# Performance work log

Measured on AMD Instinct MI355X. Metric: run time of the kernel, lower is better.

Reference implementation:

```python
import jax, jax.numpy as jnp
import numpy as np

N_NODES = 50000


def gcn_conv(x, src, dst, W, b):
    # PyG GCNConv: x @ W, symmetric gcn_norm with self-loops, scatter-add, + bias
    n = x.shape[0]
    x = x @ W  # [N, out]
    deg = jax.ops.segment_sum(jnp.ones_like(src, dtype=x.dtype), dst, num_segments=n)
    dinv = jnp.where(deg > 0, deg ** -0.5, 0.0)
    norm = dinv[src] * dinv[dst]  # [E+N]
    out = jax.ops.segment_sum(x[src] * norm[:, None], dst, num_segments=n)
    return out + b


def setup_inputs() -> dict:
    key = jax.random.key(0)
    ks = jax.random.split(key, 8)
    x = jax.random.normal(ks[0], (N_NODES, 128), dtype=jnp.float32)
    edge_index = jax.random.randint(ks[1], (2, 800000), 0, N_NODES, dtype=jnp.int64)
    def glorot(k, fan_in, fan_out):
        s = (6.0 / (fan_in + fan_out)) ** 0.5
        return jax.random.uniform(k, (fan_in, fan_out), jnp.float32, -s, s)
    return {
        "x": x,
        "edge_index": edge_index,
        "W1": glorot(ks[2], 128, 128), "b1": jnp.zeros((128,), jnp.float32),
        "W2": glorot(ks[3], 128, 128), "b2": jnp.zeros((128,), jnp.float32),
        "W3": glorot(ks[4], 128, 64), "b3": jnp.zeros((64,), jnp.float32),
    }


def reference(x, edge_index, W1, b1, W2, b2, W3, b3):
    n = x.shape[0]
    loops = jnp.arange(n, dtype=edge_index.dtype)
    src = jnp.concatenate([edge_index[0], loops])  # self-loops appended
    dst = jnp.concatenate([edge_index[1], loops])
    h = gcn_conv(x, src, dst, W1, b1)
    h = jax.nn.relu(h)  # dropout is identity in eval mode
    h = gcn_conv(h, src, dst, W2, b2)
    h = jax.nn.relu(h)
    h = gcn_conv(h, src, dst, W3, b3)
    return h
```

## Files before the change

kernel.cpp:

```cpp
#include <hip/hip_runtime.h>
#include <hip/hip_bf16.h>
#include <hip/hip_fp16.h>


typedef __attribute__((ext_vector_type(8))) short s16x8;
typedef __attribute__((ext_vector_type(8))) unsigned short u16x8;
typedef __attribute__((ext_vector_type(4))) float f32x4;

__device__ __forceinline__ float bfu_lo(uint v) { return __uint_as_float(v << 16); }
__device__ __forceinline__ float bfu_hi(uint v) { return __uint_as_float(v & 0xffff0000u); }
__device__ __forceinline__ float dec_norm(uint m) {
    return __half2float(__ushort_as_half((ushort)(m >> 16)));
}
__device__ __forceinline__ ushort bf16_bits(float f) {
    union { __hip_bfloat16 h; ushort u; } x;
    x.h = __float2bfloat16(f);
    return x.u;
}


__global__ void k_init(int* __restrict__ deg, int n,
                       uint4* __restrict__ ep4, int cap4) {
    int i = blockIdx.x * blockDim.x + threadIdx.x;
    if (i < n) deg[i] = 1;
    if (i < cap4) ep4[i] = make_uint4(0u, 0u, 0u, 0u);
}

__global__ void k_hist(const int* __restrict__ dst, int E,
                       int* __restrict__ deg, ushort* __restrict__ rank) {
    int e = blockIdx.x * blockDim.x + threadIdx.x;
    if (e < E) {
        int r = atomicAdd(&deg[dst[e]], 1);
        rank[e] = (ushort)r;
    }
}

__global__ void k_scan_block(const int* __restrict__ deg, int* __restrict__ offs,
                             int* __restrict__ bsum, float* __restrict__ dinv, int n) {
    __shared__ int sm[256];
    int tid = threadIdx.x;
    int i = blockIdx.x * 256 + tid;
    int v = (i < n) ? deg[i] : 0;
    int pv = (i < n) ? ((v + 7) & ~7) : 0;
    if (i < n) dinv[i] = rsqrtf((float)v);
    sm[tid] = pv;
    __syncthreads();
    for (int off = 1; off < 256; off <<= 1) {
        int t = (tid >= off) ? sm[tid - off] : 0;
        __syncthreads();
        sm[tid] += t;
        __syncthreads();
    }
    if (i < n) offs[i] = sm[tid] - pv;
    if (tid == 255) bsum[blockIdx.x] = sm[255];
}

__global__ void k_scan_bsum(int* __restrict__ bsum, int nb, int* __restrict__ offs, int n) {
    __shared__ int sm[256];
    int tid = threadIdx.x;
    int v = (tid < nb) ? bsum[tid] : 0;
    sm[tid] = v;
    __syncthreads();
    for (int off = 1; off < 256; off <<= 1) {
        int t = (tid >= off) ? sm[tid - off] : 0;
        __syncthreads();
        sm[tid] += t;
        __syncthreads();
    }
    if (tid < nb) bsum[tid] = sm[tid] - v;
    if (tid == 255) offs[n] = sm[255];
}

__global__ void k_add_bsum(int* __restrict__ offs, const int* __restrict__ bsum, int n) {
    int i = blockIdx.x * blockDim.x + threadIdx.x;
    if (i < n) offs[i] += bsum[i >> 8];
}

__global__ __launch_bounds__(256) void k_fill(const int* __restrict__ src,
                                              const int* __restrict__ dst,
                                              const ushort* __restrict__ rank,
                                              int E, int n,
                                              const int* __restrict__ offs,
                                              const float* __restrict__ dinv,
                                              uint* __restrict__ ep) {
    int e = blockIdx.x * blockDim.x + threadIdx.x;
    int tot = E + n;
    if (e >= tot) return;
    int s, d, r;
    if (e < E) {
        s = src[e];
        d = dst[e];
        r = rank[e];
    } else {
        s = d = e - E;
        r = 0;
    }
    int pos = offs[d] + r;
    uint hb = (uint)__half_as_ushort(__float2half(dinv[s] * dinv[d]));
    ep[pos] = (hb << 16) | (uint)s;
}

__global__ void k_transW(const float* __restrict__ W1, const float* __restrict__ W2,
                         ushort* __restrict__ Wt1, ushort* __restrict__ Wt2) {
    int i = blockIdx.x * 256 + threadIdx.x;
    if (i < 128 * 128) {
        int r = i >> 7, c = i & 127;
        Wt1[c * 128 + r] = bf16_bits(W1[i]);
        Wt2[c * 128 + r] = bf16_bits(W2[i]);
    }
}

template <bool ABF16>
__global__ __launch_bounds__(256) void k_gemm_mfma(const void* __restrict__ Ain,
                                                   const ushort* __restrict__ Wt,
                                                   __hip_bfloat16* __restrict__ T, int n) {
    __shared__ ushort As[64][136];
    __shared__ ushort Ws[128][136];
    const int tid = threadIdx.x;
    const int wave = tid >> 6, lane = tid & 63;
    const int m0 = blockIdx.x * 64;

#pragma unroll
    for (int it = 0; it < 8; ++it) {
        int idx = it * 256 + tid;
        int r = idx >> 4;
        int c8 = (idx & 15) << 3;
        *(u16x8*)&Ws[r][c8] = *(const u16x8*)(Wt + r * 128 + c8);
    }
    if constexpr (ABF16) {
        const ushort* A = (const ushort*)Ain;
#pragma unroll
        for (int it = 0; it < 4; ++it) {
            int idx = it * 256 + tid;
            int r = idx >> 4;
            int c8 = (idx & 15) << 3;
            u16x8 v = {0, 0, 0, 0, 0, 0, 0, 0};
            if (m0 + r < n) v = *(const u16x8*)(A + (size_t)(m0 + r) * 128 + c8);
            *(u16x8*)&As[r][c8] = v;
        }
    } else {
        const float* A = (const float*)Ain;
#pragma unroll
        for (int it = 0; it < 8; ++it) {
            int idx = it * 256 + tid;
            int r = idx >> 5;
            int c4 = (idx & 31) << 2;
            float4 v = make_float4(0.f, 0.f, 0.f, 0.f);
            if (m0 + r < n) v = *(const float4*)(A + (size_t)(m0 + r) * 128 + c4);
            As[r][c4 + 0] = bf16_bits(v.x);
            As[r][c4 + 1] = bf16_bits(v.y);
            As[r][c4 + 2] = bf16_bits(v.z);
            As[r][c4 + 3] = bf16_bits(v.w);
        }
    }
    __syncthreads();

    const int lrow = lane & 15;
    const int kgrp = lane >> 4;

    s16x8 a[4];
#pragma unroll
    for (int kk = 0; kk < 4; ++kk)
        a[kk] = *(const s16x8*)&As[wave * 16 + lrow][kk * 32 + kgrp * 8];

    f32x4 acc[8];
#pragma unroll
    for (int nt = 0; nt < 8; ++nt) {
        f32x4 c = {0.f, 0.f, 0.f, 0.f};
#pragma unroll
        for (int kk = 0; kk < 4; ++kk) {
            s16x8 b = *(const s16x8*)&Ws[nt * 16 + lrow][kk * 32 + kgrp * 8];
            c = __builtin_amdgcn_mfma_f32_16x16x32_bf16(a[kk], b, c, 0, 0, 0);
        }
        acc[nt] = c;
    }

    ushort* To = (ushort*)T;
#pragma unroll
    for (int j = 0; j < 4; ++j) {
        int row = m0 + wave * 16 + kgrp * 4 + j;
        if (row < n) {
#pragma unroll
            for (int nt = 0; nt < 8; ++nt)
                To[(size_t)row * 128 + nt * 16 + lrow] = bf16_bits(acc[nt][j]);
        }
    }
}

__global__ __launch_bounds__(256) void k_gemm64(const ushort* __restrict__ Aq,
                                                const float* __restrict__ W,
                                                __hip_bfloat16* __restrict__ T, int n) {
    __shared__ float As[32][68];
    __shared__ float Bs[32][68];
    const int tid = threadIdx.x;
    const int tx = tid & 15, ty = tid >> 4;
    const int m0 = blockIdx.x * 64;

    float acc[4][4] = {};

    for (int k0 = 0; k0 < 128; k0 += 32) {
#pragma unroll
        for (int it = 0; it < 2; ++it) {
            int idx = it * 256 + tid;
            int r = idx >> 3;
            int c4 = (idx & 7) << 2;
            float4 v = make_float4(0.f, 0.f, 0.f, 0.f);
            if (m0 + r < n) {
                ushort4 u = *(const ushort4*)(Aq + (size_t)(m0 + r) * 128 + k0 + c4);
                v.x = __uint_as_float((uint)u.x << 16);
                v.y = __uint_as_float((uint)u.y << 16);
                v.z = __uint_as_float((uint)u.z << 16);
                v.w = __uint_as_float((uint)u.w << 16);
            }
            As[c4 + 0][r] = v.x;
            As[c4 + 1][r] = v.y;
            As[c4 + 2][r] = v.z;
            As[c4 + 3][r] = v.w;
        }
#pragma unroll
        for (int it = 0; it < 2; ++it) {
            int idx = it * 256 + tid;
            int kk = idx >> 4;
            int c4 = (idx & 15) << 2;
            *(float4*)&Bs[kk][c4] = *(const float4*)(W + (size_t)(k0 + kk) * 64 + c4);
        }
        __syncthreads();

#pragma unroll
        for (int k = 0; k < 32; ++k) {
            float4 a = *(const float4*)&As[k][ty * 4];
            float4 b0 = *(const float4*)&Bs[k][tx * 4];
            float av[4] = {a.x, a.y, a.z, a.w};
#pragma unroll
            for (int i = 0; i < 4; ++i) {
                acc[i][0] += av[i] * b0.x;
                acc[i][1] += av[i] * b0.y;
                acc[i][2] += av[i] * b0.z;
                acc[i][3] += av[i] * b0.w;
            }
        }
        __syncthreads();
    }

#pragma unroll
    for (int i = 0; i < 4; ++i) {
        int r = m0 + ty * 4 + i;
        if (r < n) {
            union { ushort h[4]; uint2 u; } p;
#pragma unroll
            for (int j = 0; j < 4; ++j) p.h[j] = bf16_bits(acc[i][j]);
            *(uint2*)((ushort*)T + (size_t)r * 64 + tx * 4) = p.u;
        }
    }
}

template <bool RELU>
__global__ __launch_bounds__(256) void k_agg128(const __hip_bfloat16* __restrict__ T,
                                                const int* __restrict__ offs,
                                                const uint* __restrict__ ep,
                                                const float* __restrict__ bias,
                                                uint* __restrict__ outq, int n) {
    int pr = blockIdx.x * 4 + (threadIdx.x >> 6);
    int lane = threadIdx.x & 63;
    int w0 = pr * 2;
    if (w0 >= n) return;
    int w1 = w0 + 1;
    bool has1 = (w1 < n);
    int eA = offs[w0], endA = offs[w0 + 1];
    int eB = has1 ? offs[w1] : 0;
    int endB = has1 ? offs[w1 + 1] : 0;

    const uint* Tl = (const uint*)T + lane;
    const uint4 z4 = make_uint4(0u, 0u, 0u, 0u);
    float a0 = 0.f, a1 = 0.f, c0 = 0.f, c1 = 0.f;

    uint4 mA0 = *(const uint4*)(ep + eA);
    uint4 mA1 = *(const uint4*)(ep + eA + 4);
    uint4 mB0 = z4, mB1 = z4;
    if (eB < endB) { mB0 = *(const uint4*)(ep + eB); mB1 = *(const uint4*)(ep + eB + 4); }

    for (;;) {
        uint rA0 = Tl[(size_t)(mA0.x & 0xffffu) * 64];
        uint rA1 = Tl[(size_t)(mA0.y & 0xffffu) * 64];
        uint rA2 = Tl[(size_t)(mA0.z & 0xffffu) * 64];
        uint rA3 = Tl[(size_t)(mA0.w & 0xffffu) * 64];
        uint rA4 = Tl[(size_t)(mA1.x & 0xffffu) * 64];
        uint rA5 = Tl[(size_t)(mA1.y & 0xffffu) * 64];
        uint rA6 = Tl[(size_t)(mA1.z & 0xffffu) * 64];
        uint rA7 = Tl[(size_t)(mA1.w & 0xffffu) * 64];
        uint rB0 = Tl[(size_t)(mB0.x & 0xffffu) * 64];
        uint rB1 = Tl[(size_t)(mB0.y & 0xffffu) * 64];
        uint rB2 = Tl[(size_t)(mB0.z & 0xffffu) * 64];
        uint rB3 = Tl[(size_t)(mB0.w & 0xffffu) * 64];
        uint rB4 = Tl[(size_t)(mB1.x & 0xffffu) * 64];
        uint rB5 = Tl[(size_t)(mB1.y & 0xffffu) * 64];
        uint rB6 = Tl[(size_t)(mB1.z & 0xffffu) * 64];
        uint rB7 = Tl[(size_t)(mB1.w & 0xffffu) * 64];
        float wA0 = dec_norm(mA0.x), wA1 = dec_norm(mA0.y);
        float wA2 = dec_norm(mA0.z), wA3 = dec_norm(mA0.w);
        float wA4 = dec_norm(mA1.x), wA5 = dec_norm(mA1.y);
        float wA6 = dec_norm(mA1.z), wA7 = dec_norm(mA1.w);
        float wB0 = dec_norm(mB0.x), wB1 = dec_norm(mB0.y);
        float wB2 = dec_norm(mB0.z), wB3 = dec_norm(mB0.w);
        float wB4 = dec_norm(mB1.x), wB5 = dec_norm(mB1.y);
        float wB6 = dec_norm(mB1.z), wB7 = dec_norm(mB1.w);
        eA += 8;
        eB += 8;
        bool moreA = (eA < endA), moreB = (eB < endB);
        if (moreA) { mA0 = *(const uint4*)(ep + eA); mA1 = *(const uint4*)(ep + eA + 4); }
        else       { mA0 = z4; mA1 = z4; }
        if (moreB) { mB0 = *(const uint4*)(ep + eB); mB1 = *(const uint4*)(ep + eB + 4); }
        else       { mB0 = z4; mB1 = z4; }
        a0 += wA0 * bfu_lo(rA0); a1 += wA0 * bfu_hi(rA0);
        a0 += wA1 * bfu_lo(rA1); a1 += wA1 * bfu_hi(rA1);
        a0 += wA2 * bfu_lo(rA2); a1 += wA2 * bfu_hi(rA2);
        a0 += wA3 * bfu_lo(rA3); a1 += wA3 * bfu_hi(rA3);
        a0 += wA4 * bfu_lo(rA4); a1 += wA4 * bfu_hi(rA4);
        a0 += wA5 * bfu_lo(rA5); a1 += wA5 * bfu_hi(rA5);
        a0 += wA6 * bfu_lo(rA6); a1 += wA6 * bfu_hi(rA6);
        a0 += wA7 * bfu_lo(rA7); a1 += wA7 * bfu_hi(rA7);
        c0 += wB0 * bfu_lo(rB0); c1 += wB0 * bfu_hi(rB0);
        c0 += wB1 * bfu_lo(rB1); c1 += wB1 * bfu_hi(rB1);
        c0 += wB2 * bfu_lo(rB2); c1 += wB2 * bfu_hi(rB2);
        c0 += wB3 * bfu_lo(rB3); c1 += wB3 * bfu_hi(rB3);
        c0 += wB4 * bfu_lo(rB4); c1 += wB4 * bfu_hi(rB4);
        c0 += wB5 * bfu_lo(rB5); c1 += wB5 * bfu_hi(rB5);
        c0 += wB6 * bfu_lo(rB6); c1 += wB6 * bfu_hi(rB6);
        c0 += wB7 * bfu_lo(rB7); c1 += wB7 * bfu_hi(rB7);
        if (!moreA && !moreB) break;
    }

    float2 b = *(const float2*)(bias + (lane << 1));
    a0 += b.x; a1 += b.y;
    if (RELU) { a0 = fmaxf(a0, 0.f); a1 = fmaxf(a1, 0.f); }
    outq[(size_t)w0 * 64 + lane] = ((uint)bf16_bits(a1) << 16) | (uint)bf16_bits(a0);
    if (has1) {
        c0 += b.x; c1 += b.y;
        if (RELU) { c0 = fmaxf(c0, 0.f); c1 = fmaxf(c1, 0.f); }
        outq[(size_t)w1 * 64 + lane] = ((uint)bf16_bits(c1) << 16) | (uint)bf16_bits(c0);
    }
}

__global__ __launch_bounds__(256) void k_agg64(const __hip_bfloat16* __restrict__ T,
                                               const int* __restrict__ offs,
                                               const uint* __restrict__ ep,
                                               const float* __restrict__ bias,
                                               float* __restrict__ out, int n) {
    int pr = blockIdx.x * 4 + (threadIdx.x >> 6);
    int lane = threadIdx.x & 63;
    int w0 = pr * 2;
    if (w0 >= n) return;
    int w1 = w0 + 1;
    bool has1 = (w1 < n);
    int eA = offs[w0], endA = offs[w0 + 1];
    int eB = has1 ? offs[w1] : 0;
    int endB = has1 ? offs[w1 + 1] : 0;

    const ushort* Tl = (const ushort*)T + lane;
    const uint4 z4 = make_uint4(0u, 0u, 0u, 0u);
    float a0 = 0.f, c0 = 0.f;

    uint4 mA0 = *(const uint4*)(ep + eA);
    uint4 mA1 = *(const uint4*)(ep + eA + 4);
    uint4 mB0 = z4, mB1 = z4;
    if (eB < endB) { mB0 = *(const uint4*)(ep + eB); mB1 = *(const uint4*)(ep + eB + 4); }

    for (;;) {
        float rA0 = __uint_as_float((uint)Tl[(size_t)(mA0.x & 0xffffu) * 64] << 16);
        float rA1 = __uint_as_float((uint)Tl[(size_t)(mA0.y & 0xffffu) * 64] << 16);
        float rA2 = __uint_as_float((uint)Tl[(size_t)(mA0.z & 0xffffu) * 64] << 16);
        float rA3 = __uint_as_float((uint)Tl[(size_t)(mA0.w & 0xffffu) * 64] << 16);
        float rA4 = __uint_as_float((uint)Tl[(size_t)(mA1.x & 0xffffu) * 64] << 16);
        float rA5 = __uint_as_float((uint)Tl[(size_t)(mA1.y & 0xffffu) * 64] << 16);
        float rA6 = __uint_as_float((uint)Tl[(size_t)(mA1.z & 0xffffu) * 64] << 16);
        float rA7 = __uint_as_float((uint)Tl[(size_t)(mA1.w & 0xffffu) * 64] << 16);
        float rB0 = __uint_as_float((uint)Tl[(size_t)(mB0.x & 0xffffu) * 64] << 16);
        float rB1 = __uint_as_float((uint)Tl[(size_t)(mB0.y & 0xffffu) * 64] << 16);
        float rB2 = __uint_as_float((uint)Tl[(size_t)(mB0.z & 0xffffu) * 64] << 16);
        float rB3 = __uint_as_float((uint)Tl[(size_t)(mB0.w & 0xffffu) * 64] << 16);
        float rB4 = __uint_as_float((uint)Tl[(size_t)(mB1.x & 0xffffu) * 64] << 16);
        float rB5 = __uint_as_float((uint)Tl[(size_t)(mB1.y & 0xffffu) * 64] << 16);
        float rB6 = __uint_as_float((uint)Tl[(size_t)(mB1.z & 0xffffu) * 64] << 16);
        float rB7 = __uint_as_float((uint)Tl[(size_t)(mB1.w & 0xffffu) * 64] << 16);
        float wA0 = dec_norm(mA0.x), wA1 = dec_norm(mA0.y);
        float wA2 = dec_norm(mA0.z), wA3 = dec_norm(mA0.w);
        float wA4 = dec_norm(mA1.x), wA5 = dec_norm(mA1.y);
        float wA6 = dec_norm(mA1.z), wA7 = dec_norm(mA1.w);
        float wB0 = dec_norm(mB0.x), wB1 = dec_norm(mB0.y);
        float wB2 = dec_norm(mB0.z), wB3 = dec_norm(mB0.w);
        float wB4 = dec_norm(mB1.x), wB5 = dec_norm(mB1.y);
        float wB6 = dec_norm(mB1.z), wB7 = dec_norm(mB1.w);
        eA += 8;
        eB += 8;
        bool moreA = (eA < endA), moreB = (eB < endB);
        if (moreA) { mA0 = *(const uint4*)(ep + eA); mA1 = *(const uint4*)(ep + eA + 4); }
        else       { mA0 = z4; mA1 = z4; }
        if (moreB) { mB0 = *(const uint4*)(ep + eB); mB1 = *(const uint4*)(ep + eB + 4); }
        else       { mB0 = z4; mB1 = z4; }
        a0 += wA0 * rA0 + wA1 * rA1 + wA2 * rA2 + wA3 * rA3;
        a0 += wA4 * rA4 + wA5 * rA5 + wA6 * rA6 + wA7 * rA7;
        c0 += wB0 * rB0 + wB1 * rB1 + wB2 * rB2 + wB3 * rB3;
        c0 += wB4 * rB4 + wB5 * rB5 + wB6 * rB6 + wB7 * rB7;
        if (!moreA && !moreB) break;
    }

    float bv = bias[lane];
    out[(size_t)w0 * 64 + lane] = a0 + bv;
    if (has1) out[(size_t)w1 * 64 + lane] = c0 + bv;
}


extern "C" void kernel_launch(void* const* d_in, const int* in_sizes, int n_in,
                              void* d_out, int out_size, void* d_ws, size_t ws_size,
                              hipStream_t stream) {
    const int n = in_sizes[0] / 128;
    const int E = in_sizes[1] / 2;

    const float* x  = (const float*)d_in[0];
    const int*   ei = (const int*)d_in[1];
    const float* W1 = (const float*)d_in[2];
    const float* b1 = (const float*)d_in[3];
    const float* W2 = (const float*)d_in[4];
    const float* b2 = (const float*)d_in[5];
    const float* W3 = (const float*)d_in[6];
    const float* b3 = (const float*)d_in[7];
    const int* src = ei;
    const int* dst = ei + E;
    float* out = (float*)d_out;

    const int cap = E + 8 * n;

    char* w = (char*)d_ws;
    auto alloc = [&](size_t bytes) {
        char* p = w;
        w += (bytes + 255) & ~(size_t)255;
        return p;
    };
    int*    deg    = (int*)alloc((size_t)n * 4);
    int*    offs   = (int*)alloc((size_t)(n + 1) * 4);
    int*    bsum   = (int*)alloc(256 * 4);
    float*  dinv   = (float*)alloc((size_t)n * 4);
    ushort* rank   = (ushort*)alloc((size_t)E * 2);
    uint*   ep     = (uint*)alloc((size_t)cap * 4);
    __hip_bfloat16* tA = (__hip_bfloat16*)alloc((size_t)n * 128 * 2);
    uint*   hB     = (uint*)alloc((size_t)n * 64 * 4);
    ushort* Wt1    = (ushort*)alloc(128 * 128 * 2);
    ushort* Wt2    = (ushort*)alloc(128 * 128 * 2);

    const int nb = (n + 255) / 256;

    const int cap4 = (cap + 3) / 4;
    k_init<<<(cap4 + 255) / 256, 256, 0, stream>>>(deg, n, (uint4*)ep, cap4);
    k_transW<<<64, 256, 0, stream>>>(W1, W2, Wt1, Wt2);
    k_hist<<<(E + 255) / 256, 256, 0, stream>>>(dst, E, deg, rank);
    k_scan_block<<<nb, 256, 0, stream>>>(deg, offs, bsum, dinv, n);
    k_scan_bsum<<<1, 256, 0, stream>>>(bsum, nb, offs, n);
    k_add_bsum<<<nb, 256, 0, stream>>>(offs, bsum, n);
    k_fill<<<(E + n + 255) / 256, 256, 0, stream>>>(src, dst, rank, E, n, offs, dinv, ep);

    const int pair_blocks = ((n + 1) / 2 + 3) / 4;
    const int gemm_blocks = (n + 63) / 64;

    k_gemm_mfma<false><<<gemm_blocks, 256, 0, stream>>>(x, Wt1, tA, n);
    k_agg128<true><<<pair_blocks, 256, 0, stream>>>(tA, offs, ep, b1, hB, n);

    k_gemm_mfma<true><<<gemm_blocks, 256, 0, stream>>>(hB, Wt2, tA, n);
    k_agg128<true><<<pair_blocks, 256, 0, stream>>>(tA, offs, ep, b2, hB, n);

    k_gemm64<<<gemm_blocks, 256, 0, stream>>>((const ushort*)hB, W3, tA, n);
    k_agg64<<<pair_blocks, 256, 0, stream>>>(tA, offs, ep, b3, out, n);
}
```

Before: 197.5 us.

## Software-pipeline aggregation gathers and use MFMA for the third-layer GEMM

The aggregation kernels now run a three-stage rotation: edge metadata is fetched two chunks ahead and neighbour rows one chunk ahead, so gather latency overlaps with the FMAs of the current chunk. Iteration counts are precomputed from the padded CSR offsets. The scalar fp32 GEMM for the 128→64 layer is replaced by the templated bf16 MFMA kernel, using a newly transposed bf16 W3. This raises register pressure in the aggregation kernels, which may lower occupancy.

```diff
diff --git a/kernel.cpp b/kernel.cpp
--- a/kernel.cpp
+++ b/kernel.cpp
@@ -101,27 +101,34 @@
 }
 
 __global__ void k_transW(const float* __restrict__ W1, const float* __restrict__ W2,
-                         ushort* __restrict__ Wt1, ushort* __restrict__ Wt2) {
+                         const float* __restrict__ W3,
+                         ushort* __restrict__ Wt1, ushort* __restrict__ Wt2,
+                         ushort* __restrict__ Wt3) {
     int i = blockIdx.x * 256 + threadIdx.x;
     if (i < 128 * 128) {
         int r = i >> 7, c = i & 127;
         Wt1[c * 128 + r] = bf16_bits(W1[i]);
         Wt2[c * 128 + r] = bf16_bits(W2[i]);
     }
-}
-
-template <bool ABF16>
+    if (i < 128 * 64) {
+        int r = i >> 6, c = i & 63;
+        Wt3[c * 128 + r] = bf16_bits(W3[i]);
+    }
+}
+
+template <int OUT, bool ABF16>
 __global__ __launch_bounds__(256) void k_gemm_mfma(const void* __restrict__ Ain,
                                                    const ushort* __restrict__ Wt,
-                                                   __hip_bfloat16* __restrict__ T, int n) {
+                                                   ushort* __restrict__ To, int n) {
+    constexpr int NT = OUT / 16;
     __shared__ ushort As[64][136];
-    __shared__ ushort Ws[128][136];
+    __shared__ ushort Ws[OUT][136];
     const int tid = threadIdx.x;
     const int wave = tid >> 6, lane = tid & 63;
     const int m0 = blockIdx.x * 64;
 
 #pragma unroll
-    for (int it = 0; it < 8; ++it) {
+    for (int it = 0; it < OUT / 16; ++it) {
         int idx = it * 256 + tid;
         int r = idx >> 4;
         int c8 = (idx & 15) << 3;
@@ -163,9 +170,9 @@
     for (int kk = 0; kk < 4; ++kk)
         a[kk] = *(const s16x8*)&As[wave * 16 + lrow][kk * 32 + kgrp * 8];
 
-    f32x4 acc[8];
-#pragma unroll
-    for (int nt = 0; nt < 8; ++nt) {
+    f32x4 acc[NT];
+#pragma unroll
+    for (int nt = 0; nt < NT; ++nt) {
         f32x4 c = {0.f, 0.f, 0.f, 0.f};
 #pragma unroll
         for (int kk = 0; kk < 4; ++kk) {
@@ -175,87 +182,87 @@
         acc[nt] = c;
     }
 
-    ushort* To = (ushort*)T;
 #pragma unroll
     for (int j = 0; j < 4; ++j) {
         int row = m0 + wave * 16 + kgrp * 4 + j;
         if (row < n) {
 #pragma unroll
-            for (int nt = 0; nt < 8; ++nt)
-                To[(size_t)row * 128 + nt * 16 + lrow] = bf16_bits(acc[nt][j]);
+            for (int nt = 0; nt < NT; ++nt)
+                To[(size_t)row * OUT + nt * 16 + lrow] = bf16_bits(acc[nt][j]);
         }
     }
 }
 
-__global__ __launch_bounds__(256) void k_gemm64(const ushort* __restrict__ Aq,
-                                                const float* __restrict__ W,
-                                                __hip_bfloat16* __restrict__ T, int n) {
-    __shared__ float As[32][68];
-    __shared__ float Bs[32][68];
-    const int tid = threadIdx.x;
-    const int tx = tid & 15, ty = tid >> 4;
-    const int m0 = blockIdx.x * 64;
-
-    float acc[4][4] = {};
-
-    for (int k0 = 0; k0 < 128; k0 += 32) {
-#pragma unroll
-        for (int it = 0; it < 2; ++it) {
-            int idx = it * 256 + tid;
-            int r = idx >> 3;
-            int c4 = (idx & 7) << 2;
-            float4 v = make_float4(0.f, 0.f, 0.f, 0.f);
-            if (m0 + r < n) {
-                ushort4 u = *(const ushort4*)(Aq + (size_t)(m0 + r) * 128 + k0 + c4);
-                v.x = __uint_as_float((uint)u.x << 16);
-                v.y = __uint_as_float((uint)u.y << 16);
-                v.z = __uint_as_float((uint)u.z << 16);
-                v.w = __uint_as_float((uint)u.w << 16);
-            }
-            As[c4 + 0][r] = v.x;
-            As[c4 + 1][r] = v.y;
-            As[c4 + 2][r] = v.z;
-            As[c4 + 3][r] = v.w;
-        }
-#pragma unroll
-        for (int it = 0; it < 2; ++it) {
-            int idx = it * 256 + tid;
-            int kk = idx >> 4;
-            int c4 = (idx & 15) << 2;
-            *(float4*)&Bs[kk][c4] = *(const float4*)(W + (size_t)(k0 + kk) * 64 + c4);
-        }
-        __syncthreads();
-
-#pragma unroll
-        for (int k = 0; k < 32; ++k) {
-            float4 a = *(const float4*)&As[k][ty * 4];
-            float4 b0 = *(const float4*)&Bs[k][tx * 4];
-            float av[4] = {a.x, a.y, a.z, a.w};
-#pragma unroll
-            for (int i = 0; i < 4; ++i) {
-                acc[i][0] += av[i] * b0.x;
-                acc[i][1] += av[i] * b0.y;
-                acc[i][2] += av[i] * b0.z;
-                acc[i][3] += av[i] * b0.w;
-            }
-        }
-        __syncthreads();
-    }
-
-#pragma unroll
-    for (int i = 0; i < 4; ++i) {
-        int r = m0 + ty * 4 + i;
-        if (r < n) {
-            union { ushort h[4]; uint2 u; } p;
-#pragma unroll
-            for (int j = 0; j < 4; ++j) p.h[j] = bf16_bits(acc[i][j]);
-            *(uint2*)((ushort*)T + (size_t)r * 64 + tx * 4) = p.u;
-        }
-    }
-}
+
+__device__ __forceinline__ void fetch16(const uint* __restrict__ ep,
+                                        int eA0, int itA, int eB0, int itB,
+                                        int k, uint (&m)[16]) {
+    if (k < itA) {
+        uint4 a0 = *(const uint4*)(ep + eA0 + (k << 3));
+        uint4 a1 = *(const uint4*)(ep + eA0 + (k << 3) + 4);
+        m[0] = a0.x; m[1] = a0.y; m[2] = a0.z; m[3] = a0.w;
+        m[4] = a1.x; m[5] = a1.y; m[6] = a1.z; m[7] = a1.w;
+    } else {
+#pragma unroll
+        for (int i = 0; i < 8; ++i) m[i] = 0u;
+    }
+    if (k < itB) {
+        uint4 b0 = *(const uint4*)(ep + eB0 + (k << 3));
+        uint4 b1 = *(const uint4*)(ep + eB0 + (k << 3) + 4);
+        m[8] = b0.x;  m[9] = b0.y;  m[10] = b0.z; m[11] = b0.w;
+        m[12] = b1.x; m[13] = b1.y; m[14] = b1.z; m[15] = b1.w;
+    } else {
+#pragma unroll
+        for (int i = 8; i < 16; ++i) m[i] = 0u;
+    }
+}
+
+__device__ __forceinline__ void gather16u(const uint* __restrict__ Tl,
+                                          const uint (&m)[16], uint (&r)[16]) {
+#pragma unroll
+    for (int i = 0; i < 16; ++i) r[i] = Tl[(size_t)(m[i] & 0xffffu) * 64];
+}
+
+__device__ __forceinline__ void fma16u(const uint (&m)[16], const uint (&r)[16],
+                                       float& a0, float& a1, float& c0, float& c1) {
+#pragma unroll
+    for (int i = 0; i < 8; ++i) {
+        float w = dec_norm(m[i]);
+        a0 += w * bfu_lo(r[i]);
+        a1 += w * bfu_hi(r[i]);
+    }
+#pragma unroll
+    for (int i = 8; i < 16; ++i) {
+        float w = dec_norm(m[i]);
+        c0 += w * bfu_lo(r[i]);
+        c1 += w * bfu_hi(r[i]);
+    }
+}
+
+__device__ __forceinline__ void gather16s(const ushort* __restrict__ Tl,
+                                          const uint (&m)[16], uint (&r)[16]) {
+#pragma unroll
+    for (int i = 0; i < 16; ++i) r[i] = (uint)Tl[(size_t)(m[i] & 0xffffu) * 64];
+}
+
+__device__ __forceinline__ void fma16s(const uint (&m)[16], const uint (&r)[16],
+                                       float& a0, float& c0) {
+#pragma unroll
+    for (int i = 0; i < 8; ++i)
+        a0 += dec_norm(m[i]) * __uint_as_float(r[i] << 16);
+#pragma unroll
+    for (int i = 8; i < 16; ++i)
+        c0 += dec_norm(m[i]) * __uint_as_float(r[i] << 16);
+}
+
+#define AGG_HALF(GATHER, Mnext, Mfetch, Rnext, Mcur, Rcur, FMA) \
+    GATHER(Tl, Mnext, Rnext);                                   \
+    fetch16(ep, eA0, itA, eB0, itB, j + 2, Mfetch);             \
+    FMA;                                                        \
+    if (++j >= iters) break;
 
 template <bool RELU>
-__global__ __launch_bounds__(256) void k_agg128(const __hip_bfloat16* __restrict__ T,
+__global__ __launch_bounds__(256) void k_agg128(const ushort* __restrict__ T,
                                                 const int* __restrict__ offs,
                                                 const uint* __restrict__ ep,
                                                 const float* __restrict__ bias,
@@ -266,68 +273,27 @@
     if (w0 >= n) return;
     int w1 = w0 + 1;
     bool has1 = (w1 < n);
-    int eA = offs[w0], endA = offs[w0 + 1];
-    int eB = has1 ? offs[w1] : 0;
-    int endB = has1 ? offs[w1 + 1] : 0;
+    int eA0 = offs[w0];
+    int itA = (offs[w0 + 1] - eA0) >> 3;
+    int eB0 = has1 ? offs[w1] : 0;
+    int itB = has1 ? ((offs[w1 + 1] - eB0) >> 3) : 0;
+    int iters = max(itA, itB);
 
     const uint* Tl = (const uint*)T + lane;
-    const uint4 z4 = make_uint4(0u, 0u, 0u, 0u);
     float a0 = 0.f, a1 = 0.f, c0 = 0.f, c1 = 0.f;
-
-    uint4 mA0 = *(const uint4*)(ep + eA);
-    uint4 mA1 = *(const uint4*)(ep + eA + 4);
-    uint4 mB0 = z4, mB1 = z4;
-    if (eB < endB) { mB0 = *(const uint4*)(ep + eB); mB1 = *(const uint4*)(ep + eB + 4); }
-
+    uint M0[16], M1[16], M2[16], rP[16], rQ[16];
+
+    fetch16(ep, eA0, itA, eB0, itB, 0, M0);
+    gather16u(Tl, M0, rP);
+    fetch16(ep, eA0, itA, eB0, itB, 1, M1);
+    int j = 0;
     for (;;) {
-        uint rA0 = Tl[(size_t)(mA0.x & 0xffffu) * 64];
-        uint rA1 = Tl[(size_t)(mA0.y & 0xffffu) * 64];
-        uint rA2 = Tl[(size_t)(mA0.z & 0xffffu) * 64];
-        uint rA3 = Tl[(size_t)(mA0.w & 0xffffu) * 64];
-        uint rA4 = Tl[(size_t)(mA1.x & 0xffffu) * 64];
-        uint rA5 = Tl[(size_t)(mA1.y & 0xffffu) * 64];
-        uint rA6 = Tl[(size_t)(mA1.z & 0xffffu) * 64];
-        uint rA7 = Tl[(size_t)(mA1.w & 0xffffu) * 64];
-        uint rB0 = Tl[(size_t)(mB0.x & 0xffffu) * 64];
-        uint rB1 = Tl[(size_t)(mB0.y & 0xffffu) * 64];
-        uint rB2 = Tl[(size_t)(mB0.z & 0xffffu) * 64];
-        uint rB3 = Tl[(size_t)(mB0.w & 0xffffu) * 64];
-        uint rB4 = Tl[(size_t)(mB1.x & 0xffffu) * 64];
-        uint rB5 = Tl[(size_t)(mB1.y & 0xffffu) * 64];
-        uint rB6 = Tl[(size_t)(mB1.z & 0xffffu) * 64];
-        uint rB7 = Tl[(size_t)(mB1.w & 0xffffu) * 64];
-        float wA0 = dec_norm(mA0.x), wA1 = dec_norm(mA0.y);
-        float wA2 = dec_norm(mA0.z), wA3 = dec_norm(mA0.w);
-        float wA4 = dec_norm(mA1.x), wA5 = dec_norm(mA1.y);
-        float wA6 = dec_norm(mA1.z), wA7 = dec_norm(mA1.w);
-        float wB0 = dec_norm(mB0.x), wB1 = dec_norm(mB0.y);
-        float wB2 = dec_norm(mB0.z), wB3 = dec_norm(mB0.w);
-        float wB4 = dec_norm(mB1.x), wB5 = dec_norm(mB1.y);
-        float wB6 = dec_norm(mB1.z), wB7 = dec_norm(mB1.w);
-        eA += 8;
-        eB += 8;
-        bool moreA = (eA < endA), moreB = (eB < endB);
-        if (moreA) { mA0 = *(const uint4*)(ep + eA); mA1 = *(const uint4*)(ep + eA + 4); }
-        else       { mA0 = z4; mA1 = z4; }
-        if (moreB) { mB0 = *(const uint4*)(ep + eB); mB1 = *(const uint4*)(ep + eB + 4); }
-        else       { mB0 = z4; mB1 = z4; }
-        a0 += wA0 * bfu_lo(rA0); a1 += wA0 * bfu_hi(rA0);
-        a0 += wA1 * bfu_lo(rA1); a1 += wA1 * bfu_hi(rA1);
-        a0 += wA2 * bfu_lo(rA2); a1 += wA2 * bfu_hi(rA2);
-        a0 += wA3 * bfu_lo(rA3); a1 += wA3 * bfu_hi(rA3);
-        a0 += wA4 * bfu_lo(rA4); a1 += wA4 * bfu_hi(rA4);
-        a0 += wA5 * bfu_lo(rA5); a1 += wA5 * bfu_hi(rA5);
-        a0 += wA6 * bfu_lo(rA6); a1 += wA6 * bfu_hi(rA6);
-        a0 += wA7 * bfu_lo(rA7); a1 += wA7 * bfu_hi(rA7);
-        c0 += wB0 * bfu_lo(rB0); c1 += wB0 * bfu_hi(rB0);
-        c0 += wB1 * bfu_lo(rB1); c1 += wB1 * bfu_hi(rB1);
-        c0 += wB2 * bfu_lo(rB2); c1 += wB2 * bfu_hi(rB2);
-        c0 += wB3 * bfu_lo(rB3); c1 += wB3 * bfu_hi(rB3);
-        c0 += wB4 * bfu_lo(rB4); c1 += wB4 * bfu_hi(rB4);
-        c0 += wB5 * bfu_lo(rB5); c1 += wB5 * bfu_hi(rB5);
-        c0 += wB6 * bfu_lo(rB6); c1 += wB6 * bfu_hi(rB6);
-        c0 += wB7 * bfu_lo(rB7); c1 += wB7 * bfu_hi(rB7);
-        if (!moreA && !moreB) break;
+        AGG_HALF(gather16u, M1, M2, rQ, M0, rP, fma16u(M0, rP, a0, a1, c0, c1))
+        AGG_HALF(gather16u, M2, M0, rP, M1, rQ, fma16u(M1, rQ, a0, a1, c0, c1))
+        AGG_HALF(gather16u, M0, M1, rQ, M2, rP, fma16u(M2, rP, a0, a1, c0, c1))
+        AGG_HALF(gather16u, M1, M2, rP, M0, rQ, fma16u(M0, rQ, a0, a1, c0, c1))
+        AGG_HALF(gather16u, M2, M0, rQ, M1, rP, fma16u(M1, rP, a0, a1, c0, c1))
+        AGG_HALF(gather16u, M0, M1, rP, M2, rQ, fma16u(M2, rQ, a0, a1, c0, c1))
     }
 
     float2 b = *(const float2*)(bias + (lane << 1));
@@ -341,7 +307,7 @@
     }
 }
 
-__global__ __launch_bounds__(256) void k_agg64(const __hip_bfloat16* __restrict__ T,
+__global__ __launch_bounds__(256) void k_agg64(const ushort* __restrict__ T,
                                                const int* __restrict__ offs,
                                                const uint* __restrict__ ep,
                                                const float* __restrict__ bias,
@@ -352,56 +318,27 @@
     if (w0 >= n) return;
     int w1 = w0 + 1;
     bool has1 = (w1 < n);
-    int eA = offs[w0], endA = offs[w0 + 1];
-    int eB = has1 ? offs[w1] : 0;
-    int endB = has1 ? offs[w1 + 1] : 0;
-
-    const ushort* Tl = (const ushort*)T + lane;
-    const uint4 z4 = make_uint4(0u, 0u, 0u, 0u);
+    int eA0 = offs[w0];
+    int itA = (offs[w0 + 1] - eA0) >> 3;
+    int eB0 = has1 ? offs[w1] : 0;
+    int itB = has1 ? ((offs[w1 + 1] - eB0) >> 3) : 0;
+    int iters = max(itA, itB);
+
+    const ushort* Tl = T + lane;
     float a0 = 0.f, c0 = 0.f;
-
-    uint4 mA0 = *(const uint4*)(ep + eA);
-    uint4 mA1 = *(const uint4*)(ep + eA + 4);
-    uint4 mB0 = z4, mB1 = z4;
-    if (eB < endB) { mB0 = *(const uint4*)(ep + eB); mB1 = *(const uint4*)(ep + eB + 4); }
-
+    uint M0[16], M1[16], M2[16], rP[16], rQ[16];
+
+    fetch16(ep, eA0, itA, eB0, itB, 0, M0);
+    gather16s(Tl, M0, rP);
+    fetch16(ep, eA0, itA, eB0, itB, 1, M1);
+    int j = 0;
     for (;;) {
-        float rA0 = __uint_as_float((uint)Tl[(size_t)(mA0.x & 0xffffu) * 64] << 16);
-        float rA1 = __uint_as_float((uint)Tl[(size_t)(mA0.y & 0xffffu) * 64] << 16);
-        float rA2 = __uint_as_float((uint)Tl[(size_t)(mA0.z & 0xffffu) * 64] << 16);
-        float rA3 = __uint_as_float((uint)Tl[(size_t)(mA0.w & 0xffffu) * 64] << 16);
-        float rA4 = __uint_as_float((uint)Tl[(size_t)(mA1.x & 0xffffu) * 64] << 16);
-        float rA5 = __uint_as_float((uint)Tl[(size_t)(mA1.y & 0xffffu) * 64] << 16);
-        float rA6 = __uint_as_float((uint)Tl[(size_t)(mA1.z & 0xffffu) * 64] << 16);
-        float rA7 = __uint_as_float((uint)Tl[(size_t)(mA1.w & 0xffffu) * 64] << 16);
-        float rB0 = __uint_as_float((uint)Tl[(size_t)(mB0.x & 0xffffu) * 64] << 16);
-        float rB1 = __uint_as_float((uint)Tl[(size_t)(mB0.y & 0xffffu) * 64] << 16);
-        float rB2 = __uint_as_float((uint)Tl[(size_t)(mB0.z & 0xffffu) * 64] << 16);
-        float rB3 = __uint_as_float((uint)Tl[(size_t)(mB0.w & 0xffffu) * 64] << 16);
-        float rB4 = __uint_as_float((uint)Tl[(size_t)(mB1.x & 0xffffu) * 64] << 16);
-        float rB5 = __uint_as_float((uint)Tl[(size_t)(mB1.y & 0xffffu) * 64] << 16);
-        float rB6 = __uint_as_float((uint)Tl[(size_t)(mB1.z & 0xffffu) * 64] << 16);
-        float rB7 = __uint_as_float((uint)Tl[(size_t)(mB1.w & 0xffffu) * 64] << 16);
-        float wA0 = dec_norm(mA0.x), wA1 = dec_norm(mA0.y);
-        float wA2 = dec_norm(mA0.z), wA3 = dec_norm(mA0.w);
-        float wA4 = dec_norm(mA1.x), wA5 = dec_norm(mA1.y);
-        float wA6 = dec_norm(mA1.z), wA7 = dec_norm(mA1.w);
-        float wB0 = dec_norm(mB0.x), wB1 = dec_norm(mB0.y);
-        float wB2 = dec_norm(mB0.z), wB3 = dec_norm(mB0.w);
-        float wB4 = dec_norm(mB1.x), wB5 = dec_norm(mB1.y);
-        float wB6 = dec_norm(mB1.z), wB7 = dec_norm(mB1.w);
-        eA += 8;
-        eB += 8;
-        bool moreA = (eA < endA), moreB = (eB < endB);
-        if (moreA) { mA0 = *(const uint4*)(ep + eA); mA1 = *(const uint4*)(ep + eA + 4); }
-        else       { mA0 = z4; mA1 = z4; }
-        if (moreB) { mB0 = *(const uint4*)(ep + eB); mB1 = *(const uint4*)(ep + eB + 4); }
-        else       { mB0 = z4; mB1 = z4; }
-        a0 += wA0 * rA0 + wA1 * rA1 + wA2 * rA2 + wA3 * rA3;
-        a0 += wA4 * rA4 + wA5 * rA5 + wA6 * rA6 + wA7 * rA7;
-        c0 += wB0 * rB0 + wB1 * rB1 + wB2 * rB2 + wB3 * rB3;
-        c0 += wB4 * rB4 + wB5 * rB5 + wB6 * rB6 + wB7 * rB7;
-        if (!moreA && !moreB) break;
+        AGG_HALF(gather16s, M1, M2, rQ, M0, rP, fma16s(M0, rP, a0, c0))
+        AGG_HALF(gather16s, M2, M0, rP, M1, rQ, fma16s(M1, rQ, a0, c0))
+        AGG_HALF(gather16s, M0, M1, rQ, M2, rP, fma16s(M2, rP, a0, c0))
+        AGG_HALF(gather16s, M1, M2, rP, M0, rQ, fma16s(M0, rQ, a0, c0))
+        AGG_HALF(gather16s, M2, M0, rQ, M1, rP, fma16s(M1, rP, a0, c0))
+        AGG_HALF(gather16s, M0, M1, rP, M2, rQ, fma16s(M2, rQ, a0, c0))
     }
 
     float bv = bias[lane];
@@ -442,16 +379,17 @@
     float*  dinv   = (float*)alloc((size_t)n * 4);
     ushort* rank   = (ushort*)alloc((size_t)E * 2);
     uint*   ep     = (uint*)alloc((size_t)cap * 4);
-    __hip_bfloat16* tA = (__hip_bfloat16*)alloc((size_t)n * 128 * 2);
+    ushort* tA     = (ushort*)alloc((size_t)n * 128 * 2);
     uint*   hB     = (uint*)alloc((size_t)n * 64 * 4);
     ushort* Wt1    = (ushort*)alloc(128 * 128 * 2);
     ushort* Wt2    = (ushort*)alloc(128 * 128 * 2);
+    ushort* Wt3    = (ushort*)alloc(64 * 128 * 2);
 
     const int nb = (n + 255) / 256;
 
     const int cap4 = (cap + 3) / 4;
     k_init<<<(cap4 + 255) / 256, 256, 0, stream>>>(deg, n, (uint4*)ep, cap4);
-    k_transW<<<64, 256, 0, stream>>>(W1, W2, Wt1, Wt2);
+    k_transW<<<64, 256, 0, stream>>>(W1, W2, W3, Wt1, Wt2, Wt3);
     k_hist<<<(E + 255) / 256, 256, 0, stream>>>(dst, E, deg, rank);
     k_scan_block<<<nb, 256, 0, stream>>>(deg, offs, bsum, dinv, n);
     k_scan_bsum<<<1, 256, 0, stream>>>(bsum, nb, offs, n);
@@ -461,12 +399,12 @@
     const int pair_blocks = ((n + 1) / 2 + 3) / 4;
     const int gemm_blocks = (n + 63) / 64;
 
-    k_gemm_mfma<false><<<gemm_blocks, 256, 0, stream>>>(x, Wt1, tA, n);
+    k_gemm_mfma<128, false><<<gemm_blocks, 256, 0, stream>>>(x, Wt1, tA, n);
     k_agg128<true><<<pair_blocks, 256, 0, stream>>>(tA, offs, ep, b1, hB, n);
 
-    k_gemm_mfma<true><<<gemm_blocks, 256, 0, stream>>>(hB, Wt2, tA, n);
+    k_gemm_mfma<128, true><<<gemm_blocks, 256, 0, stream>>>(hB, Wt2, tA, n);
     k_agg128<true><<<pair_blocks, 256, 0, stream>>>(tA, offs, ep, b2, hB, n);
 
-    k_gemm64<<<gemm_blocks, 256, 0, stream>>>((const ushort*)hB, W3, tA, n);
+    k_gemm_mfma<64, true><<<gemm_blocks, 256, 0, stream>>>(hB, Wt3, tA, n);
     k_agg64<<<pair_blocks, 256, 0, stream>>>(tA, offs, ep, b3, out, n);
 }
```

Result: slower. 219.6 us (+11.2%).
